# Kernel optimization log

Hardware: AMD Instinct MI355X
Metric: run time of the kernel (lower is better)

## Reference

```python
import jax, jax.numpy as jnp
import numpy as np

B, L, D, H = 4, 2048, 1024, 16
d = D // H  # head_dim = 64
EPS = 1e-5
ROPE_BASE = 10000.0


def _rope_tables(seq_len, dim):
    inv_freq = 1.0 / (ROPE_BASE ** (jnp.arange(0, dim, 2, dtype=jnp.float32) / dim))
    t = jnp.arange(seq_len, dtype=jnp.float32)
    freqs = jnp.outer(t, inv_freq)                  # (L, d/2)
    emb = jnp.concatenate([freqs, freqs], axis=-1)  # (L, d)
    return jnp.cos(emb), jnp.sin(emb)


def _rotate_half(x):
    x1, x2 = jnp.split(x, 2, axis=-1)
    return jnp.concatenate([-x2, x1], axis=-1)


def setup_inputs() -> dict:
    key = jax.random.key(0)
    ks = jax.random.split(key, 5)
    x = jax.random.normal(ks[0], (B, L, D), dtype=jnp.float32)
    attn_mask = jnp.ones((B, 1, L, L), dtype=jnp.float32)
    conversion_mask = jax.random.uniform(ks[1], (B, L), dtype=jnp.float32)
    Wqkuv = jax.random.normal(ks[2], (D, 4 * D), dtype=jnp.float32) * (1.0 / np.sqrt(D))
    Wout = jax.random.normal(ks[3], (D, D), dtype=jnp.float32) * (1.0 / np.sqrt(D))
    ln_gamma = jnp.ones((d,), dtype=jnp.float32)
    ln_beta = jnp.zeros((d,), dtype=jnp.float32)
    conv_bias = jax.random.normal(ks[4], (H,), dtype=jnp.float32) * 0.02
    return {"x": x, "attn_mask": attn_mask, "conversion_mask": conversion_mask,
            "Wqkuv": Wqkuv, "Wout": Wout, "ln_gamma": ln_gamma,
            "ln_beta": ln_beta, "conv_bias": conv_bias}


def reference(x, attn_mask, conversion_mask, Wqkuv, Wout, ln_gamma, ln_beta, conv_bias):
    # qkuv projection with SiLU
    qkuv = jax.nn.silu(jnp.einsum('bld,de->ble', x, Wqkuv))  # (B, L, 4D)
    q, k, v, u = jnp.split(qkuv, 4, axis=-1)
    # reshape to (B, H, L, d)
    to_heads = lambda t: t.reshape(B, L, H, d).transpose(0, 2, 1, 3)
    q, k, v, u = map(to_heads, (q, k, v, u))
    # RoPE
    cos, sin = _rope_tables(L, d)            # (L, d)
    cos = cos[None, None]                    # (1,1,L,d)
    sin = sin[None, None]
    q = q * cos + _rotate_half(q) * sin
    k = k * cos + _rotate_half(k) * sin
    # scores + conversion bias + SiLU + multiplicative mask
    scores = jnp.einsum('bhld,bhmd->bhlm', q, k) / jnp.sqrt(jnp.float32(d))
    scores = scores + conversion_mask[:, None, None, :] * conv_bias[None, :, None, None]
    scores = jax.nn.silu(scores)
    scores = scores * attn_mask
    # attend, LayerNorm over head_dim, SiLU-gate with u
    attn_out = jnp.einsum('bhlm,bhmd->bhld', scores, v)
    mu = jnp.mean(attn_out, axis=-1, keepdims=True)
    var = jnp.var(attn_out, axis=-1, keepdims=True)
    attn_out = (attn_out - mu) / jnp.sqrt(var + EPS) * ln_gamma + ln_beta
    attn_out = attn_out * u
    attn_out = attn_out.transpose(0, 2, 1, 3).reshape(B, L, D)
    return jnp.einsum('bld,de->ble', attn_out, Wout)
```

## Files before the change

### kernel.cpp

```cpp
#include <hip/hip_runtime.h>
#include <math.h>
#include <stdint.h>

#define B_ 4
#define L_ 2048
#define D_ 1024
#define H_ 16

typedef __attribute__((ext_vector_type(4))) float f32x4;
typedef __attribute__((ext_vector_type(2))) float f32x2;
typedef __attribute__((ext_vector_type(8))) short s16x8;
typedef __attribute__((ext_vector_type(4))) short s16x4;
typedef __attribute__((ext_vector_type(4))) unsigned short u16x4;
typedef __attribute__((ext_vector_type(4))) unsigned int u32x4;
typedef __attribute__((ext_vector_type(2))) __bf16 bf16x2;

__device__ __forceinline__ unsigned short f2bf(float f) {
  unsigned int u = __float_as_uint(f);
  u += 0x7fffu + ((u >> 16) & 1u);
  return (unsigned short)(u >> 16);
}
__device__ __forceinline__ float b2f(unsigned short s) {
  return __uint_as_float(((unsigned int)s) << 16);
}
__device__ __forceinline__ unsigned int pk2(float a, float b) {
  f32x2 v;
  v[0] = a;
  v[1] = b;
  bf16x2 r = __builtin_convertvector(v, bf16x2);
  return __builtin_bit_cast(unsigned int, r);
}
__device__ __forceinline__ float silu_fast(float v) {
  return v * __builtin_amdgcn_rcpf(1.0f + __expf(-v));
}
__device__ __forceinline__ void gl_lds16(const void* g, void* l) {
  __builtin_amdgcn_global_load_lds(
      (__attribute__((address_space(1))) void*)(uintptr_t)g,
      (__attribute__((address_space(3))) void*)(uint32_t)(uintptr_t)l, 16, 0, 0);
}

__global__ __launch_bounds__(256) void conv_x(const float* __restrict__ x,
                                              unsigned short* __restrict__ xb, int n4) {
  int i = blockIdx.x * 256 + threadIdx.x;
  if (i < n4) {
    f32x4 v = *(const f32x4*)(x + (size_t)i * 4);
    u16x4 o;
#pragma unroll
    for (int j = 0; j < 4; ++j) o[j] = f2bf(v[j]);
    *(u16x4*)(xb + (size_t)i * 4) = o;
  }
}

__global__ __launch_bounds__(256) void trans_w(const float* __restrict__ W,
                                               unsigned short* __restrict__ Wt,
                                               int K, int N) {
  __shared__ float T[64][65];
  const int k0 = blockIdx.y * 64, n0 = blockIdx.x * 64;
  const int tid = threadIdx.x;
#pragma unroll
  for (int i = 0; i < 16; ++i) {
    int e = tid + i * 256;
    int r = e >> 6, c = e & 63;
    T[r][c] = W[(size_t)(k0 + r) * N + n0 + c];
  }
  __syncthreads();
#pragma unroll
  for (int i = 0; i < 16; ++i) {
    int e = tid + i * 256;
    int r = e >> 6, c = e & 63;
    Wt[(size_t)(n0 + r) * K + k0 + c] = f2bf(T[c][r]);
  }
}

__global__ __launch_bounds__(256) void rope_tab(f32x2* __restrict__ tab) {
  int i = blockIdx.x * 256 + threadIdx.x;
  int l = i >> 5, j = i & 31;
  float inv = expf(-(float)j * (9.210340371976184f / 32.0f));
  float ang = (float)l * inv;
  f32x2 cs;
  cs[0] = cosf(ang);
  cs[1] = sinf(ang);
  tab[i] = cs;
}

template <int MODE>
__global__ __launch_bounds__(256) void gemm_bf16(const unsigned short* __restrict__ A,
                                                 const unsigned short* __restrict__ Bt,
                                                 void* __restrict__ Cp,
                                                 int M, int N, int K) {
  alignas(16) __shared__ unsigned short As[128][32];
  alignas(16) __shared__ unsigned short Bs[128][32];
  const int tid = threadIdx.x;
  const int lane = tid & 63, w = tid >> 6;
  const int quad = lane >> 4, l15 = lane & 15;
  const int wr = w >> 1, wc = w & 1;
  const int nwg = gridDim.x * gridDim.y;
  const int wgid = blockIdx.y * gridDim.x + blockIdx.x;
  const int swz = (wgid & 7) * (nwg >> 3) + (wgid >> 3);
  const int m0 = (swz / gridDim.x) * 128, n0 = (swz % gridDim.x) * 128;
  const int srow = lane >> 2;
  const int schunk = (lane & 3) ^ ((lane >> 3) & 3);
  const int fcol = (quad ^ ((l15 >> 1) & 3)) * 8;
  f32x4 acc[4][4] = {};
  for (int k0 = 0; k0 < K; k0 += 32) {
    __syncthreads();
#pragma unroll
    for (int i = 0; i < 2; ++i) {
      int r0 = (w * 2 + i) * 16;
      gl_lds16(A + (size_t)(m0 + r0 + srow) * K + k0 + schunk * 8, &As[r0][0]);
      gl_lds16(Bt + (size_t)(n0 + r0 + srow) * K + k0 + schunk * 8, &Bs[r0][0]);
    }
    __syncthreads();
    s16x8 af[4], bf[4];
#pragma unroll
    for (int mi = 0; mi < 4; ++mi) af[mi] = *(const s16x8*)&As[wr * 64 + mi * 16 + l15][fcol];
#pragma unroll
    for (int nj = 0; nj < 4; ++nj) bf[nj] = *(const s16x8*)&Bs[wc * 64 + nj * 16 + l15][fcol];
#pragma unroll
    for (int mi = 0; mi < 4; ++mi)
#pragma unroll
      for (int nj = 0; nj < 4; ++nj)
        acc[mi][nj] = __builtin_amdgcn_mfma_f32_16x16x32_bf16(af[mi], bf[nj], acc[mi][nj], 0, 0, 0);
  }
#pragma unroll
  for (int mi = 0; mi < 4; ++mi)
#pragma unroll
    for (int nj = 0; nj < 4; ++nj)
#pragma unroll
      for (int reg = 0; reg < 4; ++reg) {
        int rg = m0 + wr * 64 + mi * 16 + quad * 4 + reg;
        int cg = n0 + wc * 64 + nj * 16 + l15;
        float v = acc[mi][nj][reg];
        if (MODE == 1) {
          ((unsigned short*)Cp)[(size_t)rg * N + cg] = f2bf(silu_fast(v));
        } else {
          ((float*)Cp)[(size_t)rg * N + cg] = v;
        }
      }
}

__global__ __launch_bounds__(256) void rope_conv(unsigned short* __restrict__ qk,
                                                 unsigned short* __restrict__ vt,
                                                 const f32x2* __restrict__ tab) {
  alignas(16) __shared__ unsigned short Vsh[64][72];
  const int tid = threadIdx.x;
  const int bh = blockIdx.y, b = bh >> 4, h = bh & 15;
  const int l0 = blockIdx.x * 64;
#pragma unroll
  for (int i = 0; i < 2; ++i) {
    int p = tid + i * 256;
    int row = p >> 3, c4 = p & 7;
    int l = l0 + row;
    size_t base = (size_t)(b * L_ + l) * 4096 + h * 64 + c4 * 4;
#pragma unroll
    for (int t = 0; t < 2; ++t) {
      size_t o = base + (size_t)t * 1024;
      u16x4 lo = *(u16x4*)(qk + o);
      u16x4 hi = *(u16x4*)(qk + o + 32);
      u16x4 nlo, nhi;
#pragma unroll
      for (int jj = 0; jj < 4; ++jj) {
        f32x2 cs = tab[l * 32 + c4 * 4 + jj];
        float fl = b2f(lo[jj]), fh = b2f(hi[jj]);
        nlo[jj] = f2bf(fl * cs[0] - fh * cs[1]);
        nhi[jj] = f2bf(fh * cs[0] + fl * cs[1]);
      }
      *(u16x4*)(qk + o) = nlo;
      *(u16x4*)(qk + o + 32) = nhi;
    }
  }
#pragma unroll
  for (int i = 0; i < 2; ++i) {
    int ch = tid + i * 256;
    int row = ch >> 3, c8 = ch & 7;
    *(s16x8*)&Vsh[row][c8 * 8] =
        *(const s16x8*)(qk + (size_t)(b * L_ + l0 + row) * 4096 + 2048 + h * 64 + c8 * 8);
  }
  __syncthreads();
#pragma unroll
  for (int i = 0; i < 2; ++i) {
    int ch = tid + i * 256;
    int drow = ch >> 3, c8 = ch & 7;
    s16x8 o;
#pragma unroll
    for (int jj = 0; jj < 8; ++jj) {
      int pos = c8 * 8 + jj;
      int g = pos >> 5, p = pos & 31;
      int lk = g * 32 + ((p >> 2) & 1) * 16 + ((p >> 3) & 3) * 4 + (p & 3);
      o[jj] = (short)Vsh[lk][drow];
    }
    *(s16x8*)(vt + (size_t)(bh * 64 + drow) * 2048 + l0 + c8 * 8) = o;
  }
}

__global__ __launch_bounds__(256) void attn_mfma(
    const unsigned short* __restrict__ qk, const unsigned short* __restrict__ vt,
    const float* __restrict__ amask, const float* __restrict__ cmask,
    const float* __restrict__ cbias, const float* __restrict__ gamma,
    const float* __restrict__ beta, unsigned short* __restrict__ attng) {
  alignas(16) __shared__ unsigned short Ks[64][64];
  alignas(16) __shared__ unsigned short Vts[64][64];
  const int tid = threadIdx.x;
  const int lane = tid & 63, w = tid >> 6;
  const int quad = lane >> 4, l15 = lane & 15;
  const int wgid = blockIdx.y * 32 + blockIdx.x;
  const int swz = (wgid & 7) * 256 + (wgid >> 3);
  const int bh = swz >> 5, b = bh >> 4, h = bh & 15;
  const int l0 = (swz & 31) * 64;
  const float cb = cbias[h];
  const int srow = lane >> 3;
  const int schunk = (lane & 7) ^ srow;

  s16x8 qf[2];
  const int qg = l0 + w * 16 + l15;
#pragma unroll
  for (int s = 0; s < 2; ++s)
    qf[s] = *(const s16x8*)(qk + (size_t)(b * L_ + qg) * 4096 + h * 64 + s * 32 + quad * 8);
  const float* abase = amask + ((size_t)b * L_ + qg) * L_;
  const float* cbase = cmask + (size_t)b * L_;

  f32x4 oacc[4] = {};

  for (int m0 = 0; m0 < L_; m0 += 64) {
    __syncthreads();
#pragma unroll
    for (int i = 0; i < 2; ++i) {
      int r0 = w * 16 + i * 8;
      gl_lds16(qk + (size_t)(b * L_ + m0 + r0 + srow) * 4096 + 1024 + h * 64 + schunk * 8,
               &Ks[r0][0]);
      gl_lds16(vt + (size_t)(bh * 64 + r0 + srow) * 2048 + m0 + schunk * 8, &Vts[r0][0]);
    }
    f32x4 cmcb[4], am4[4];
#pragma unroll
    for (int kt = 0; kt < 4; ++kt)
      cmcb[kt] = *(const f32x4*)(cbase + m0 + kt * 16 + quad * 4) * cb;
#pragma unroll
    for (int kt = 0; kt < 4; ++kt)
      am4[kt] = *(const f32x4*)(abase + m0 + kt * 16 + quad * 4);
    __syncthreads();

    f32x4 sacc[4] = {};
#pragma unroll
    for (int s = 0; s < 2; ++s) {
      s16x8 kf[4];
#pragma unroll
      for (int kt = 0; kt < 4; ++kt)
        kf[kt] = *(const s16x8*)&Ks[kt * 16 + l15][((s * 4 + quad) ^ (l15 & 7)) * 8];
      __builtin_amdgcn_s_setprio(1);
#pragma unroll
      for (int kt = 0; kt < 4; ++kt)
        sacc[kt] = __builtin_amdgcn_mfma_f32_16x16x32_bf16(kf[kt], qf[s], sacc[kt], 0, 0, 0);
      __builtin_amdgcn_s_setprio(0);
    }

    s16x8 pf[2];
#pragma unroll
    for (int t = 0; t < 2; ++t) {
      u32x4 pw;
#pragma unroll
      for (int half = 0; half < 2; ++half) {
        int kt = 2 * t + half;
        float x[4];
#pragma unroll
        for (int r = 0; r < 4; ++r) {
          float v = fmaf(sacc[kt][r], 0.125f, cmcb[kt][r]);
          v = silu_fast(v);
          x[r] = v * am4[kt][r];
        }
        pw[half * 2 + 0] = pk2(x[0], x[1]);
        pw[half * 2 + 1] = pk2(x[2], x[3]);
      }
      pf[t] = __builtin_bit_cast(s16x8, pw);
    }

#pragma unroll
    for (int dt = 0; dt < 4; ++dt)
#pragma unroll
      for (int t = 0; t < 2; ++t) {
        s16x8 vf = *(const s16x8*)&Vts[dt * 16 + l15][((t * 4 + quad) ^ (l15 & 7)) * 8];
        __builtin_amdgcn_s_setprio(1);
        oacc[dt] = __builtin_amdgcn_mfma_f32_16x16x32_bf16(pf[t], vf, oacc[dt], 0, 0, 0);
        __builtin_amdgcn_s_setprio(0);
      }
  }

  {
    float sm[4], sq[4];
#pragma unroll
    for (int reg = 0; reg < 4; ++reg) {
      float s1 = 0.f, s2 = 0.f;
#pragma unroll
      for (int dt = 0; dt < 4; ++dt) {
        float v = oacc[dt][reg];
        s1 += v;
        s2 += v * v;
      }
      sm[reg] = s1;
      sq[reg] = s2;
    }
#pragma unroll
    for (int m = 1; m < 16; m <<= 1) {
#pragma unroll
      for (int reg = 0; reg < 4; ++reg) {
        sm[reg] += __shfl_xor(sm[reg], m);
        sq[reg] += __shfl_xor(sq[reg], m);
      }
    }
    float mu[4], rs[4];
#pragma unroll
    for (int reg = 0; reg < 4; ++reg) {
      mu[reg] = sm[reg] * (1.0f / 64.0f);
      float var = sq[reg] * (1.0f / 64.0f) - mu[reg] * mu[reg];
      rs[reg] = rsqrtf(var + 1e-5f);
    }
#pragma unroll
    for (int dt = 0; dt < 4; ++dt) {
      float g = gamma[dt * 16 + l15], be = beta[dt * 16 + l15];
#pragma unroll
      for (int reg = 0; reg < 4; ++reg) {
        int rowg = l0 + w * 16 + quad * 4 + reg;
        int colg = dt * 16 + l15;
        float v = (oacc[dt][reg] - mu[reg]) * rs[reg] * g + be;
        float u = b2f(qk[(size_t)(b * L_ + rowg) * 4096 + 3072 + h * 64 + colg]);
        attng[(size_t)(b * L_ + rowg) * 1024 + h * 64 + colg] = f2bf(v * u);
      }
    }
  }
}

extern "C" void kernel_launch(void* const* d_in, const int* in_sizes, int n_in,
                              void* d_out, int out_size, void* d_ws, size_t ws_size,
                              hipStream_t stream) {
  const float* x = (const float*)d_in[0];
  const float* amask = (const float*)d_in[1];
  const float* cmask = (const float*)d_in[2];
  const float* Wqkuv = (const float*)d_in[3];
  const float* Wout = (const float*)d_in[4];
  const float* gamma = (const float*)d_in[5];
  const float* beta = (const float*)d_in[6];
  const float* cbias = (const float*)d_in[7];
  float* out = (float*)d_out;

  char* ws = (char*)d_ws;
  unsigned short* qkuv_bf = (unsigned short*)ws;
  unsigned short* vt = (unsigned short*)(ws + ((size_t)64 << 20));
  unsigned short* xbf = (unsigned short*)(ws + ((size_t)80 << 20));
  unsigned short* Wt = (unsigned short*)(ws + ((size_t)96 << 20));
  unsigned short* Wot = (unsigned short*)(ws + ((size_t)104 << 20));
  unsigned short* attng = (unsigned short*)(ws + ((size_t)106 << 20));
  f32x2* tab = (f32x2*)(ws + ((size_t)122 << 20));

  conv_x<<<8192, 256, 0, stream>>>(x, xbf, (B_ * L_ * D_) / 4);
  trans_w<<<dim3(4096 / 64, 1024 / 64), 256, 0, stream>>>(Wqkuv, Wt, 1024, 4096);
  trans_w<<<dim3(1024 / 64, 1024 / 64), 256, 0, stream>>>(Wout, Wot, 1024, 1024);
  rope_tab<<<(L_ * 32) / 256, 256, 0, stream>>>(tab);

  gemm_bf16<1><<<dim3(4096 / 128, 8192 / 128), 256, 0, stream>>>(xbf, Wt, qkuv_bf,
                                                                 B_ * L_, 4 * D_, D_);
  rope_conv<<<dim3(L_ / 64, B_ * H_), 256, 0, stream>>>(qkuv_bf, vt, tab);
  attn_mfma<<<dim3(L_ / 64, B_ * H_), 256, 0, stream>>>(qkuv_bf, vt, amask, cmask, cbias,
                                                        gamma, beta, attng);
  gemm_bf16<0><<<dim3(1024 / 128, 8192 / 128), 256, 0, stream>>>(attng, Wot, out,
                                                                 B_ * L_, D_, D_);
}
```

Measured before the change: 481.9 us.

## Double-buffer K/V tiles in LDS and software-pipeline QK^T with PV

The attention loop is rewritten as a two-stage software pipeline with double-buffered K and V shared-memory tiles. The next K tile's QK^T MFMAs now overlap the current tile's SiLU epilogue and PV MFMAs, and global-to-LDS loads are issued one step ahead, so each iteration waits on fewer load stalls. Mask loads are also shifted to overlap with compute. The workgroup-index swizzle is dropped in favour of direct blockIdx mapping, which may change L2 locality. The cost is double the LDS and more live registers (two score accumulators), which could reduce occupancy.

After: 488.2 us. Within noise of the previous version (+1.3%).

```diff
diff --git a/kernel.cpp b/kernel.cpp
--- a/kernel.cpp
+++ b/kernel.cpp
@@ -198,15 +198,13 @@
     const float* __restrict__ amask, const float* __restrict__ cmask,
     const float* __restrict__ cbias, const float* __restrict__ gamma,
     const float* __restrict__ beta, unsigned short* __restrict__ attng) {
-  alignas(16) __shared__ unsigned short Ks[64][64];
-  alignas(16) __shared__ unsigned short Vts[64][64];
+  alignas(16) __shared__ unsigned short Kb[2][64][64];
+  alignas(16) __shared__ unsigned short Vb[2][64][64];
   const int tid = threadIdx.x;
   const int lane = tid & 63, w = tid >> 6;
   const int quad = lane >> 4, l15 = lane & 15;
-  const int wgid = blockIdx.y * 32 + blockIdx.x;
-  const int swz = (wgid & 7) * 256 + (wgid >> 3);
-  const int bh = swz >> 5, b = bh >> 4, h = bh & 15;
-  const int l0 = (swz & 31) * 64;
+  const int bh = blockIdx.y, b = bh >> 4, h = bh & 15;
+  const int l0 = blockIdx.x * 64;
   const float cb = cbias[h];
   const int srow = lane >> 3;
   const int schunk = (lane & 7) ^ srow;
@@ -220,40 +218,40 @@
   const float* cbase = cmask + (size_t)b * L_;
 
   f32x4 oacc[4] = {};
-
-  for (int m0 = 0; m0 < L_; m0 += 64) {
-    __syncthreads();
+  f32x4 cmcb[4], am4[4];
+
+  auto stageK = [&](int slot, int m0) {
 #pragma unroll
     for (int i = 0; i < 2; ++i) {
       int r0 = w * 16 + i * 8;
       gl_lds16(qk + (size_t)(b * L_ + m0 + r0 + srow) * 4096 + 1024 + h * 64 + schunk * 8,
-               &Ks[r0][0]);
-      gl_lds16(vt + (size_t)(bh * 64 + r0 + srow) * 2048 + m0 + schunk * 8, &Vts[r0][0]);
-    }
-    f32x4 cmcb[4], am4[4];
-#pragma unroll
-    for (int kt = 0; kt < 4; ++kt)
-      cmcb[kt] = *(const f32x4*)(cbase + m0 + kt * 16 + quad * 4) * cb;
-#pragma unroll
-    for (int kt = 0; kt < 4; ++kt)
-      am4[kt] = *(const f32x4*)(abase + m0 + kt * 16 + quad * 4);
-    __syncthreads();
-
-    f32x4 sacc[4] = {};
+               &Kb[slot][r0][0]);
+    }
+  };
+  auto stageV = [&](int slot, int m0) {
+#pragma unroll
+    for (int i = 0; i < 2; ++i) {
+      int r0 = w * 16 + i * 8;
+      gl_lds16(vt + (size_t)(bh * 64 + r0 + srow) * 2048 + m0 + schunk * 8, &Vb[slot][r0][0]);
+    }
+  };
+  auto qkt = [&](int slot, f32x4 (&sacc)[4]) {
+#pragma unroll
+    for (int kt = 0; kt < 4; ++kt) sacc[kt] = f32x4{0.f, 0.f, 0.f, 0.f};
 #pragma unroll
     for (int s = 0; s < 2; ++s) {
       s16x8 kf[4];
 #pragma unroll
       for (int kt = 0; kt < 4; ++kt)
-        kf[kt] = *(const s16x8*)&Ks[kt * 16 + l15][((s * 4 + quad) ^ (l15 & 7)) * 8];
+        kf[kt] = *(const s16x8*)&Kb[slot][kt * 16 + l15][((s * 4 + quad) ^ (l15 & 7)) * 8];
       __builtin_amdgcn_s_setprio(1);
 #pragma unroll
       for (int kt = 0; kt < 4; ++kt)
         sacc[kt] = __builtin_amdgcn_mfma_f32_16x16x32_bf16(kf[kt], qf[s], sacc[kt], 0, 0, 0);
       __builtin_amdgcn_s_setprio(0);
     }
-
-    s16x8 pf[2];
+  };
+  auto epi = [&](const f32x4 (&sacc)[4], s16x8 (&pf)[2]) {
 #pragma unroll
     for (int t = 0; t < 2; ++t) {
       u32x4 pw;
@@ -272,16 +270,71 @@
       }
       pf[t] = __builtin_bit_cast(s16x8, pw);
     }
-
+  };
+  auto ldmasks = [&](int m0) {
+#pragma unroll
+    for (int kt = 0; kt < 4; ++kt) {
+      cmcb[kt] = *(const f32x4*)(cbase + m0 + kt * 16 + quad * 4) * cb;
+      am4[kt] = *(const f32x4*)(abase + m0 + kt * 16 + quad * 4);
+    }
+  };
+  auto pv = [&](int slot, const s16x8 (&pf)[2]) {
 #pragma unroll
     for (int dt = 0; dt < 4; ++dt)
 #pragma unroll
       for (int t = 0; t < 2; ++t) {
-        s16x8 vf = *(const s16x8*)&Vts[dt * 16 + l15][((t * 4 + quad) ^ (l15 & 7)) * 8];
+        s16x8 vf = *(const s16x8*)&Vb[slot][dt * 16 + l15][((t * 4 + quad) ^ (l15 & 7)) * 8];
         __builtin_amdgcn_s_setprio(1);
         oacc[dt] = __builtin_amdgcn_mfma_f32_16x16x32_bf16(pf[t], vf, oacc[dt], 0, 0, 0);
         __builtin_amdgcn_s_setprio(0);
       }
+  };
+
+  f32x4 sA[4], sB[4];
+
+  stageK(0, 0);
+  __syncthreads();
+  stageK(1, 64);
+  stageV(0, 0);
+  qkt(0, sA);
+  ldmasks(0);
+  for (int p = 0; p < 15; ++p) {
+    const int i = 1 + 2 * p;
+    __syncthreads();
+    stageK(0, (i + 1) * 64);
+    stageV(1, i * 64);
+    qkt(1, sB);
+    {
+      s16x8 pf[2];
+      epi(sA, pf);
+      ldmasks(i * 64);
+      pv(0, pf);
+    }
+    __syncthreads();
+    stageK(1, (i + 2) * 64);
+    stageV(0, (i + 1) * 64);
+    qkt(0, sA);
+    {
+      s16x8 pf[2];
+      epi(sB, pf);
+      ldmasks((i + 1) * 64);
+      pv(1, pf);
+    }
+  }
+  __syncthreads();
+  stageV(1, 31 * 64);
+  qkt(1, sB);
+  {
+    s16x8 pf[2];
+    epi(sA, pf);
+    ldmasks(31 * 64);
+    pv(0, pf);
+  }
+  __syncthreads();
+  {
+    s16x8 pf[2];
+    epi(sB, pf);
+    pv(1, pf);
   }
 
   {
```
